# Kernel tuning notes

Measured on AMD Instinct MI355X. Metric: run time of the kernel, lower is better.

Reference implementation:

```python
import jax, jax.numpy as jnp
import numpy as np

NUM_HEADS = 8
MASK_RATE = 0.5


def setup_inputs() -> dict:
    key = jax.random.key(0)
    ks = jax.random.split(key, 6)
    B, N, C = 8, 1024, 256
    TABLE = 10
    att_embedding = jax.random.normal(ks[0], (B, N, C), dtype=jnp.float32)
    relation_position = jax.random.randint(ks[1], (B, N, N), 0, TABLE, dtype=jnp.int32)
    rel_len = jax.random.randint(ks[2], (B,), 0, 20, dtype=jnp.int32)
    W_qkv = jax.random.normal(ks[3], (C, 3 * C), dtype=jnp.float32) * (1.0 / np.sqrt(C))
    W_proj = jax.random.normal(ks[4], (C, C), dtype=jnp.float32) * (1.0 / np.sqrt(C))
    b_proj = jnp.zeros((C,), dtype=jnp.float32)
    bias_table = jax.random.normal(ks[5], (TABLE, NUM_HEADS), dtype=jnp.float32) * 0.02
    return {
        "att_embedding": att_embedding,
        "relation_position": relation_position,
        "rel_len": rel_len,
        "W_qkv": W_qkv,
        "W_proj": W_proj,
        "b_proj": b_proj,
        "bias_table": bias_table,
    }


def reference(att_embedding, relation_position, rel_len, W_qkv, W_proj, b_proj, bias_table):
    B, N, C = att_embedding.shape
    H = NUM_HEADS
    hd = C // H
    scale = hd ** -0.5

    # QKV projection (no bias): [B,N,3C] -> q,k,v each [B,H,N,hd]
    qkv = (att_embedding @ W_qkv).reshape(B, N, 3, H, hd)
    qkv = jnp.transpose(qkv, (2, 0, 3, 1, 4))
    q, k, v = qkv[0], qkv[1], qkv[2]

    # Attention scores [B,H,N,N]
    attn = jnp.einsum("bhnd,bhmd->bhnm", q, k) * scale

    # Relative position bias: gather [B,N,N,H] -> [B,H,N,N]
    pos_bias = jnp.transpose(bias_table[relation_position], (0, 3, 1, 2))

    # Mask bias: table row t gets -100 iff t > mask_len (mask_len+1 .. TABLE-1);
    # identical across heads -> compute as [B,1,N,N] instead of materializing [B,H,N,N].
    mask_len = (rel_len.astype(jnp.float32) * MASK_RATE).astype(jnp.int32)
    mask_bias = jnp.where(relation_position > mask_len[:, None, None], -100.0, 0.0)[:, None]

    attn = jax.nn.softmax(attn + pos_bias + mask_bias, axis=-1)

    # Weighted values -> [B,N,C] -> output projection
    x = jnp.einsum("bhnm,bhmd->bnhd", attn, v).reshape(B, N, C)
    x = x @ W_proj + b_proj
    return x
```

## Files before the change

### kernel.cpp

```cpp
#include <hip/hip_runtime.h>
#include <hip/hip_bf16.h>

typedef __bf16 bf16;
typedef __bf16 bf16x2 __attribute__((ext_vector_type(2)));
typedef __bf16 bf16x8 __attribute__((ext_vector_type(8)));
typedef float f32x4 __attribute__((ext_vector_type(4)));
typedef int i32x4 __attribute__((ext_vector_type(4)));

#define B_ 8
#define N_ 1024
#define C_ 256
#define H_ 8
#define C3_ 768
#define SCALE 0.17677669529663689f
#define FMAX 16.0f


__global__ __launch_bounds__(256) void prep(
    const float* __restrict__ Wqkv, const float* __restrict__ Wproj,
    bf16* __restrict__ Wq_tiled, bf16* __restrict__ Wp_tiled)
{
  int bb = blockIdx.x;
  int o = bb * 256 + threadIdx.x;
  if (bb < 768) {
    int kk = o & 31;
    int idx = o >> 5;
    int nr = idx & 63;
    int qq = idx >> 6;
    int nt = qq % 12, kt = qq / 12;
    int n = nt * 64 + nr, k = kt * 32 + kk;
    Wq_tiled[o] = (bf16)Wqkv[k * C3_ + n];
  } else {
    int p = o - 768 * 256;
    int kk = p & 31;
    int n = (p >> 5) & 255;
    int kt = p >> 13;
    int k = kt * 32 + kk;
    Wp_tiled[p] = (bf16)Wproj[k * C_ + n];
  }
}

__global__ __launch_bounds__(256) void gemm_qkv(
    const float* __restrict__ A, const bf16* __restrict__ Wq_tiled,
    bf16* __restrict__ q, bf16* __restrict__ kT, bf16* __restrict__ vT)
{
  __shared__ bf16 As[128][40];
  __shared__ bf16 Bts[128][40];
  __shared__ bf16 Vls[64][136];

  int tid = threadIdx.x;
  int wave = tid >> 6, lane = tid & 63, quad = lane >> 4, l16 = lane & 15;
  int m0 = blockIdx.x * 128, n0 = blockIdx.y * 128;
  int msub = (wave & 1) * 64, nsub = (wave >> 1) * 64;

  f32x4 acc[4][4] = {};

  int arow = tid >> 1, akc = (tid & 1) * 16;
  const float* aptr = A + (long)(m0 + arow) * C_ + akc;
  int bn = tid >> 1, bkc = (tid & 1) * 16;
  const bf16* bptr = Wq_tiled +
      ((long)(blockIdx.y * 2 + (bn >> 6)) * 2048 + (bn & 63) * 32 + bkc);

  float4 a0 = *reinterpret_cast<const float4*>(aptr);
  float4 a1 = *reinterpret_cast<const float4*>(aptr + 4);
  float4 a2 = *reinterpret_cast<const float4*>(aptr + 8);
  float4 a3 = *reinterpret_cast<const float4*>(aptr + 12);
  i32x4 bv0 = *reinterpret_cast<const i32x4*>(bptr);
  i32x4 bv1 = *reinterpret_cast<const i32x4*>(bptr + 8);

  for (int kt = 0; kt < 8; ++kt) {
    __syncthreads();
    {
      bf16 at[16] = {(bf16)a0.x, (bf16)a0.y, (bf16)a0.z, (bf16)a0.w,
                     (bf16)a1.x, (bf16)a1.y, (bf16)a1.z, (bf16)a1.w,
                     (bf16)a2.x, (bf16)a2.y, (bf16)a2.z, (bf16)a2.w,
                     (bf16)a3.x, (bf16)a3.y, (bf16)a3.z, (bf16)a3.w};
      *reinterpret_cast<bf16x8*>(&As[arow][akc]) = *reinterpret_cast<bf16x8*>(at);
      *reinterpret_cast<bf16x8*>(&As[arow][akc + 8]) = *reinterpret_cast<bf16x8*>(at + 8);
      *reinterpret_cast<i32x4*>(&Bts[bn][bkc]) = bv0;
      *reinterpret_cast<i32x4*>(&Bts[bn][bkc + 8]) = bv1;
    }
    __syncthreads();

    if (kt < 7) {
      int kn = (kt + 1) * 32;
      a0 = *reinterpret_cast<const float4*>(aptr + kn);
      a1 = *reinterpret_cast<const float4*>(aptr + kn + 4);
      a2 = *reinterpret_cast<const float4*>(aptr + kn + 8);
      a3 = *reinterpret_cast<const float4*>(aptr + kn + 12);
      bv0 = *reinterpret_cast<const i32x4*>(bptr + (long)(kt + 1) * 24576);
      bv1 = *reinterpret_cast<const i32x4*>(bptr + (long)(kt + 1) * 24576 + 8);
    }

    bf16x8 af[4], bfr[4];
#pragma unroll
    for (int mi = 0; mi < 4; ++mi)
      af[mi] = *reinterpret_cast<const bf16x8*>(&As[msub + mi * 16 + l16][quad * 8]);
#pragma unroll
    for (int ni = 0; ni < 4; ++ni)
      bfr[ni] = *reinterpret_cast<const bf16x8*>(&Bts[nsub + ni * 16 + l16][quad * 8]);
#pragma unroll
    for (int mi = 0; mi < 4; ++mi)
#pragma unroll
      for (int ni = 0; ni < 4; ++ni)
        acc[mi][ni] = __builtin_amdgcn_mfma_f32_16x16x32_bf16(af[mi], bfr[ni], acc[mi][ni], 0, 0, 0);
  }

  if (n0 < 256) {
#pragma unroll
    for (int mi = 0; mi < 4; ++mi)
#pragma unroll
      for (int ni = 0; ni < 4; ++ni)
#pragma unroll
        for (int r = 0; r < 4; ++r) {
          int row = m0 + msub + mi * 16 + quad * 4 + r;
          int col = n0 + nsub + ni * 16 + l16;
          q[(long)row * 256 + col] = (bf16)(acc[mi][ni][r] * SCALE);
        }
  } else if (n0 < 512) {
#pragma unroll
    for (int mi = 0; mi < 4; ++mi)
#pragma unroll
      for (int ni = 0; ni < 4; ++ni)
#pragma unroll
        for (int r = 0; r < 4; ++r) {
          int row = m0 + msub + mi * 16 + quad * 4 + r;
          int c = n0 + nsub + ni * 16 + l16 - 256;
          int b = row >> 10, n = row & 1023;
          int h = c >> 5, d = c & 31;
          kT[(((long)(b * H_ + h)) * N_ + n) * 32 + d] = (bf16)acc[mi][ni][r];
        }
  } else {
    int b = m0 >> 10;
#pragma unroll
    for (int ch = 0; ch < 2; ++ch) {
      __syncthreads();
      if ((nsub >> 6) == ch) {
#pragma unroll
        for (int mi = 0; mi < 4; ++mi)
#pragma unroll
          for (int ni = 0; ni < 4; ++ni)
#pragma unroll
            for (int r = 0; r < 4; ++r) {
              int cc = ni * 16 + l16;
              int nn = msub + mi * 16 + quad * 4 + r;
              int np = (nn & 96) | (2 * (nn & 15)) | ((nn >> 4) & 1);
              Vls[cc][np] = (bf16)acc[mi][ni][r];
            }
      }
      __syncthreads();
      int cc = tid >> 2, nseg = (tid & 3) * 32;
      long base = ((long)(b * C_ + (n0 - 512) + ch * 64 + cc)) * N_ + (m0 & 1023) + nseg;
#pragma unroll
      for (int j = 0; j < 4; ++j)
        *reinterpret_cast<i32x4*>(vT + base + j * 8) =
            *reinterpret_cast<const i32x4*>(&Vls[cc][nseg + j * 8]);
    }
  }
}

__global__ __launch_bounds__(512) void flash_attn(
    const bf16* __restrict__ q, const bf16* __restrict__ kT,
    const bf16* __restrict__ vT, const int* __restrict__ rel,
    const int* __restrict__ rel_len, const float* __restrict__ btab,
    const bf16* __restrict__ Wp_tiled, const float* __restrict__ bias,
    float* __restrict__ out)
{
  __shared__ bf16 Vs[256][40];
  __shared__ unsigned RelsP[4][33];
  __shared__ bf16 Pls[H_][16 * 40];
  __shared__ float btl[H_][16];
  __shared__ bf16 attL[16][264];

  int tid = threadIdx.x;
  int h = tid >> 6, lane = tid & 63, quad = lane >> 4, l16 = lane & 15;
  int b = blockIdx.y, i0 = blockIdx.x * 16;
  long bN = (long)b * N_;

  int mask_len = (int)((float)rel_len[b] * 0.5f);
  if (tid < 80) {
    int t = tid >> 3, hh = tid & 7;
    btl[hh][t] = btab[t * H_ + hh] + (t > mask_len ? -100.f : 0.f) - FMAX;
  }

  bf16x8 qf = *reinterpret_cast<const bf16x8*>(
      q + (bN + i0 + l16) * 256 + h * 32 + quad * 8);

  const bf16* kbase = kT + ((long)(b * H_ + h)) * N_ * 32 + quad * 8;
  int vrow = tid >> 1, voff = (tid & 1) * 16;
  const bf16* vgp = vT + ((long)b * C_ + vrow) * N_ + voff;
  int rg = (tid >> 5) & 3, rcol = tid & 31;
  const int* rgp = rel + (bN + i0 + rg * 4) * N_ + rcol;

  bf16x8 kf0 = *reinterpret_cast<const bf16x8*>(kbase + (long)l16 * 32);
  bf16x8 kf1 = *reinterpret_cast<const bf16x8*>(kbase + (long)(16 + l16) * 32);
  bf16x8 vr0 = *reinterpret_cast<const bf16x8*>(vgp);
  bf16x8 vr1 = *reinterpret_cast<const bf16x8*>(vgp + 8);
  int rr0 = 0, rr1 = 0, rr2 = 0, rr3 = 0;
  if (tid < 128) {
    rr0 = rgp[0]; rr1 = rgp[N_]; rr2 = rgp[2 * N_]; rr3 = rgp[3 * N_];
  }

  f32x4 oacc[2] = {};
  float l_part[4] = {0.f, 0.f, 0.f, 0.f};

  for (int j0 = 0; j0 < N_; j0 += 32) {
    __syncthreads();
    *reinterpret_cast<bf16x8*>(&Vs[vrow][voff]) = vr0;
    *reinterpret_cast<bf16x8*>(&Vs[vrow][voff + 8]) = vr1;
    if (tid < 128)
      RelsP[rg][rcol] = (unsigned)rr0 | ((unsigned)rr1 << 8) |
                        ((unsigned)rr2 << 16) | ((unsigned)rr3 << 24);
    __syncthreads();

    int jn = j0 + 32; jn = (jn < N_) ? jn : 0;
    bf16x8 kn0 = *reinterpret_cast<const bf16x8*>(kbase + (long)(jn + l16) * 32);
    bf16x8 kn1 = *reinterpret_cast<const bf16x8*>(kbase + (long)(jn + 16 + l16) * 32);
    vr0 = *reinterpret_cast<const bf16x8*>(vgp + jn);
    vr1 = *reinterpret_cast<const bf16x8*>(vgp + jn + 8);
    if (tid < 128) {
      rr0 = rgp[jn]; rr1 = rgp[N_ + jn];
      rr2 = rgp[2 * N_ + jn]; rr3 = rgp[3 * N_ + jn];
    }

    f32x4 z = {};
    f32x4 s0 = __builtin_amdgcn_mfma_f32_16x16x32_bf16(qf, kf0, z, 0, 0, 0);
    f32x4 s1 = __builtin_amdgcn_mfma_f32_16x16x32_bf16(qf, kf1, z, 0, 0, 0);
    kf0 = kn0; kf1 = kn1;

    unsigned w0 = RelsP[quad][l16];
    unsigned w1 = RelsP[quad][16 + l16];
#pragma unroll
    for (int r = 0; r < 4; ++r) {
      int il = quad * 4 + r;
      int rv0 = (w0 >> (8 * r)) & 255;
      int rv1 = (w1 >> (8 * r)) & 255;
      float p0 = __expf(s0[r] + btl[h][rv0]);
      float p1 = __expf(s1[r] + btl[h][rv1]);
      l_part[r] += p0 + p1;
      bf16x2 pp = {(bf16)p0, (bf16)p1};
      *reinterpret_cast<bf16x2*>(&Pls[h][il * 40 + l16 * 2]) = pp;
    }
    asm volatile("s_waitcnt lgkmcnt(0)" ::: "memory");
    bf16x8 pf = *reinterpret_cast<const bf16x8*>(&Pls[h][l16 * 40 + quad * 8]);
    bf16x8 vf0 = *reinterpret_cast<const bf16x8*>(&Vs[h * 32 + l16][quad * 8]);
    bf16x8 vf1 = *reinterpret_cast<const bf16x8*>(&Vs[h * 32 + 16 + l16][quad * 8]);
    oacc[0] = __builtin_amdgcn_mfma_f32_16x16x32_bf16(pf, vf0, oacc[0], 0, 0, 0);
    oacc[1] = __builtin_amdgcn_mfma_f32_16x16x32_bf16(pf, vf1, oacc[1], 0, 0, 0);
  }

#pragma unroll
  for (int r = 0; r < 4; ++r) {
    float l = l_part[r];
#pragma unroll
    for (int m = 1; m < 16; m <<= 1) l += __shfl_xor(l, m);
    float inv = 1.f / l;
    attL[quad * 4 + r][h * 32 + l16] = (bf16)(oacc[0][r] * inv);
    attL[quad * 4 + r][h * 32 + 16 + l16] = (bf16)(oacc[1][r] * inv);
  }
  __syncthreads();

  f32x4 pacc[2] = {};
  const bf16* wp = Wp_tiled + ((h * 32 + l16) * 32 + quad * 8);
#pragma unroll
  for (int kt = 0; kt < 8; ++kt) {
    bf16x8 afr = *reinterpret_cast<const bf16x8*>(&attL[l16][kt * 32 + quad * 8]);
    bf16x8 b0 = *reinterpret_cast<const bf16x8*>(wp + kt * 8192);
    bf16x8 b1 = *reinterpret_cast<const bf16x8*>(wp + kt * 8192 + 512);
    pacc[0] = __builtin_amdgcn_mfma_f32_16x16x32_bf16(afr, b0, pacc[0], 0, 0, 0);
    pacc[1] = __builtin_amdgcn_mfma_f32_16x16x32_bf16(afr, b1, pacc[1], 0, 0, 0);
  }
  float bi0 = bias[h * 32 + l16];
  float bi1 = bias[h * 32 + 16 + l16];
#pragma unroll
  for (int r = 0; r < 4; ++r) {
    long rowoff = (bN + i0 + quad * 4 + r) * C_ + h * 32;
    out[rowoff + l16] = pacc[0][r] + bi0;
    out[rowoff + 16 + l16] = pacc[1][r] + bi1;
  }
}

extern "C" void kernel_launch(void* const* d_in, const int* in_sizes, int n_in,
                              void* d_out, int out_size, void* d_ws, size_t ws_size,
                              hipStream_t stream) {
  const float* X     = (const float*)d_in[0];
  const int*   rel   = (const int*)d_in[1];
  const int*   rlen  = (const int*)d_in[2];
  const float* Wqkv  = (const float*)d_in[3];
  const float* Wproj = (const float*)d_in[4];
  const float* bproj = (const float*)d_in[5];
  const float* btab  = (const float*)d_in[6];
  float* out = (float*)d_out;

  char* ws = (char*)d_ws;
  bf16* Wq_tiled = (bf16*)ws;
  bf16* Wp_tiled = (bf16*)(ws + 393216);
  bf16* q  = (bf16*)(ws + 524288);
  bf16* kT = (bf16*)(ws + 524288 + 4194304);
  bf16* vT = (bf16*)(ws + 524288 + 2 * 4194304);

  prep<<<dim3(1024), 256, 0, stream>>>(Wqkv, Wproj, Wq_tiled, Wp_tiled);
  gemm_qkv<<<dim3(8192 / 128, C3_ / 128), 256, 0, stream>>>(X, Wq_tiled, q, kT, vT);
  flash_attn<<<dim3(N_ / 16, B_), 512, 0, stream>>>(
      q, kT, vT, rel, rlen, btab, Wp_tiled, bproj, out);
}
```

Before: 140.1 us.

## Halve QKV GEMM N-tile, fold log2e into scale, replicate bias LUT, coalesce prep

After: 151.0 us. 1.08x slower.

```diff
diff --git a/kernel.cpp b/kernel.cpp
--- a/kernel.cpp
+++ b/kernel.cpp
@@ -12,7 +12,7 @@
 #define C_ 256
 #define H_ 8
 #define C3_ 768
-#define SCALE 0.17677669529663689f
+#define QS 0.25500398f
 #define FMAX 16.0f
 
 
@@ -20,23 +20,17 @@
     const float* __restrict__ Wqkv, const float* __restrict__ Wproj,
     bf16* __restrict__ Wq_tiled, bf16* __restrict__ Wp_tiled)
 {
-  int bb = blockIdx.x;
-  int o = bb * 256 + threadIdx.x;
-  if (bb < 768) {
-    int kk = o & 31;
-    int idx = o >> 5;
-    int nr = idx & 63;
-    int qq = idx >> 6;
-    int nt = qq % 12, kt = qq / 12;
-    int n = nt * 64 + nr, k = kt * 32 + kk;
-    Wq_tiled[o] = (bf16)Wqkv[k * C3_ + n];
+  int o = blockIdx.x * 256 + threadIdx.x;
+  if (blockIdx.x < 768) {
+    int k = o / C3_, n = o % C3_;
+    float v = Wqkv[o];
+    int kt = k >> 5, kk = k & 31, nt = n >> 6, nr = n & 63;
+    Wq_tiled[kt * 24576 + nt * 2048 + nr * 32 + kk] = (bf16)v;
   } else {
     int p = o - 768 * 256;
-    int kk = p & 31;
-    int n = (p >> 5) & 255;
-    int kt = p >> 13;
-    int k = kt * 32 + kk;
-    Wp_tiled[p] = (bf16)Wproj[k * C_ + n];
+    int k = p >> 8, n = p & 255;
+    float v = Wproj[p];
+    Wp_tiled[(k >> 5) * 8192 + n * 32 + (k & 31)] = (bf16)v;
   }
 }
 
@@ -45,28 +39,26 @@
     bf16* __restrict__ q, bf16* __restrict__ kT, bf16* __restrict__ vT)
 {
   __shared__ bf16 As[128][40];
-  __shared__ bf16 Bts[128][40];
+  __shared__ bf16 Bts[64][40];
   __shared__ bf16 Vls[64][136];
 
   int tid = threadIdx.x;
   int wave = tid >> 6, lane = tid & 63, quad = lane >> 4, l16 = lane & 15;
-  int m0 = blockIdx.x * 128, n0 = blockIdx.y * 128;
-  int msub = (wave & 1) * 64, nsub = (wave >> 1) * 64;
-
-  f32x4 acc[4][4] = {};
+  int m0 = blockIdx.x * 128, by = blockIdx.y;
+  int msub = (wave & 1) * 64, nsub = (wave >> 1) * 32;
+
+  f32x4 acc[4][2] = {};
 
   int arow = tid >> 1, akc = (tid & 1) * 16;
   const float* aptr = A + (long)(m0 + arow) * C_ + akc;
-  int bn = tid >> 1, bkc = (tid & 1) * 16;
-  const bf16* bptr = Wq_tiled +
-      ((long)(blockIdx.y * 2 + (bn >> 6)) * 2048 + (bn & 63) * 32 + bkc);
+  int bn = tid >> 2, bkc = (tid & 3) * 8;
+  const bf16* bptr = Wq_tiled + ((long)by * 2048 + bn * 32 + bkc);
 
   float4 a0 = *reinterpret_cast<const float4*>(aptr);
   float4 a1 = *reinterpret_cast<const float4*>(aptr + 4);
   float4 a2 = *reinterpret_cast<const float4*>(aptr + 8);
   float4 a3 = *reinterpret_cast<const float4*>(aptr + 12);
-  i32x4 bv0 = *reinterpret_cast<const i32x4*>(bptr);
-  i32x4 bv1 = *reinterpret_cast<const i32x4*>(bptr + 8);
+  i32x4 bv = *reinterpret_cast<const i32x4*>(bptr);
 
   for (int kt = 0; kt < 8; ++kt) {
     __syncthreads();
@@ -77,8 +69,7 @@
                      (bf16)a3.x, (bf16)a3.y, (bf16)a3.z, (bf16)a3.w};
       *reinterpret_cast<bf16x8*>(&As[arow][akc]) = *reinterpret_cast<bf16x8*>(at);
       *reinterpret_cast<bf16x8*>(&As[arow][akc + 8]) = *reinterpret_cast<bf16x8*>(at + 8);
-      *reinterpret_cast<i32x4*>(&Bts[bn][bkc]) = bv0;
-      *reinterpret_cast<i32x4*>(&Bts[bn][bkc + 8]) = bv1;
+      *reinterpret_cast<i32x4*>(&Bts[bn][bkc]) = bv;
     }
     __syncthreads();
 
@@ -88,74 +79,68 @@
       a1 = *reinterpret_cast<const float4*>(aptr + kn + 4);
       a2 = *reinterpret_cast<const float4*>(aptr + kn + 8);
       a3 = *reinterpret_cast<const float4*>(aptr + kn + 12);
-      bv0 = *reinterpret_cast<const i32x4*>(bptr + (long)(kt + 1) * 24576);
-      bv1 = *reinterpret_cast<const i32x4*>(bptr + (long)(kt + 1) * 24576 + 8);
-    }
-
-    bf16x8 af[4], bfr[4];
+      bv = *reinterpret_cast<const i32x4*>(bptr + (long)(kt + 1) * 24576);
+    }
+
+    bf16x8 af[4], bfr[2];
 #pragma unroll
     for (int mi = 0; mi < 4; ++mi)
       af[mi] = *reinterpret_cast<const bf16x8*>(&As[msub + mi * 16 + l16][quad * 8]);
 #pragma unroll
-    for (int ni = 0; ni < 4; ++ni)
+    for (int ni = 0; ni < 2; ++ni)
       bfr[ni] = *reinterpret_cast<const bf16x8*>(&Bts[nsub + ni * 16 + l16][quad * 8]);
 #pragma unroll
     for (int mi = 0; mi < 4; ++mi)
 #pragma unroll
-      for (int ni = 0; ni < 4; ++ni)
+      for (int ni = 0; ni < 2; ++ni)
         acc[mi][ni] = __builtin_amdgcn_mfma_f32_16x16x32_bf16(af[mi], bfr[ni], acc[mi][ni], 0, 0, 0);
   }
 
-  if (n0 < 256) {
-#pragma unroll
-    for (int mi = 0; mi < 4; ++mi)
-#pragma unroll
-      for (int ni = 0; ni < 4; ++ni)
+  if (by < 4) {
+#pragma unroll
+    for (int mi = 0; mi < 4; ++mi)
+#pragma unroll
+      for (int ni = 0; ni < 2; ++ni)
 #pragma unroll
         for (int r = 0; r < 4; ++r) {
           int row = m0 + msub + mi * 16 + quad * 4 + r;
-          int col = n0 + nsub + ni * 16 + l16;
-          q[(long)row * 256 + col] = (bf16)(acc[mi][ni][r] * SCALE);
+          int col = by * 64 + nsub + ni * 16 + l16;
+          q[(long)row * 256 + col] = (bf16)(acc[mi][ni][r] * QS);
         }
-  } else if (n0 < 512) {
-#pragma unroll
-    for (int mi = 0; mi < 4; ++mi)
-#pragma unroll
-      for (int ni = 0; ni < 4; ++ni)
+  } else if (by < 8) {
+#pragma unroll
+    for (int mi = 0; mi < 4; ++mi)
+#pragma unroll
+      for (int ni = 0; ni < 2; ++ni)
 #pragma unroll
         for (int r = 0; r < 4; ++r) {
           int row = m0 + msub + mi * 16 + quad * 4 + r;
-          int c = n0 + nsub + ni * 16 + l16 - 256;
+          int c = (by - 4) * 64 + nsub + ni * 16 + l16;
           int b = row >> 10, n = row & 1023;
           int h = c >> 5, d = c & 31;
           kT[(((long)(b * H_ + h)) * N_ + n) * 32 + d] = (bf16)acc[mi][ni][r];
         }
   } else {
     int b = m0 >> 10;
-#pragma unroll
-    for (int ch = 0; ch < 2; ++ch) {
-      __syncthreads();
-      if ((nsub >> 6) == ch) {
-#pragma unroll
-        for (int mi = 0; mi < 4; ++mi)
-#pragma unroll
-          for (int ni = 0; ni < 4; ++ni)
-#pragma unroll
-            for (int r = 0; r < 4; ++r) {
-              int cc = ni * 16 + l16;
-              int nn = msub + mi * 16 + quad * 4 + r;
-              int np = (nn & 96) | (2 * (nn & 15)) | ((nn >> 4) & 1);
-              Vls[cc][np] = (bf16)acc[mi][ni][r];
-            }
-      }
-      __syncthreads();
-      int cc = tid >> 2, nseg = (tid & 3) * 32;
-      long base = ((long)(b * C_ + (n0 - 512) + ch * 64 + cc)) * N_ + (m0 & 1023) + nseg;
-#pragma unroll
-      for (int j = 0; j < 4; ++j)
-        *reinterpret_cast<i32x4*>(vT + base + j * 8) =
-            *reinterpret_cast<const i32x4*>(&Vls[cc][nseg + j * 8]);
-    }
+    __syncthreads();
+#pragma unroll
+    for (int mi = 0; mi < 4; ++mi)
+#pragma unroll
+      for (int ni = 0; ni < 2; ++ni)
+#pragma unroll
+        for (int r = 0; r < 4; ++r) {
+          int cc = nsub + ni * 16 + l16;
+          int nn = msub + mi * 16 + quad * 4 + r;
+          int np = (nn & 96) | (2 * (nn & 15)) | ((nn >> 4) & 1);
+          Vls[cc][np] = (bf16)acc[mi][ni][r];
+        }
+    __syncthreads();
+    int cc = tid >> 2, nseg = (tid & 3) * 32;
+    long base = ((long)(b * C_ + (by - 8) * 64 + cc)) * N_ + (m0 & 1023) + nseg;
+#pragma unroll
+    for (int j = 0; j < 4; ++j)
+      *reinterpret_cast<i32x4*>(vT + base + j * 8) =
+          *reinterpret_cast<const i32x4*>(&Vls[cc][nseg + j * 8]);
   }
 }
 
@@ -169,7 +154,7 @@
   __shared__ bf16 Vs[256][40];
   __shared__ unsigned RelsP[4][33];
   __shared__ bf16 Pls[H_][16 * 40];
-  __shared__ float btl[H_][16];
+  __shared__ float btlq[4][H_][17];
   __shared__ bf16 attL[16][264];
 
   int tid = threadIdx.x;
@@ -178,9 +163,10 @@
   long bN = (long)b * N_;
 
   int mask_len = (int)((float)rel_len[b] * 0.5f);
-  if (tid < 80) {
-    int t = tid >> 3, hh = tid & 7;
-    btl[hh][t] = btab[t * H_ + hh] + (t > mask_len ? -100.f : 0.f) - FMAX;
+  if (tid < 320) {
+    int cp = tid / 80, rem = tid % 80, t = rem >> 3, hh = rem & 7;
+    btlq[cp][hh][t] =
+        (btab[t * H_ + hh] + (t > mask_len ? -100.f : 0.f) - FMAX) * 1.44269504f;
   }
 
   bf16x8 qf = *reinterpret_cast<const bf16x8*>(
@@ -235,8 +221,8 @@
       int il = quad * 4 + r;
       int rv0 = (w0 >> (8 * r)) & 255;
       int rv1 = (w1 >> (8 * r)) & 255;
-      float p0 = __expf(s0[r] + btl[h][rv0]);
-      float p1 = __expf(s1[r] + btl[h][rv1]);
+      float p0 = exp2f(s0[r] + btlq[quad][h][rv0]);
+      float p1 = exp2f(s1[r] + btlq[quad][h][rv1]);
       l_part[r] += p0 + p1;
       bf16x2 pp = {(bf16)p0, (bf16)p1};
       *reinterpret_cast<bf16x2*>(&Pls[h][il * 40 + l16 * 2]) = pp;
@@ -300,7 +286,7 @@
   bf16* vT = (bf16*)(ws + 524288 + 2 * 4194304);
 
   prep<<<dim3(1024), 256, 0, stream>>>(Wqkv, Wproj, Wq_tiled, Wp_tiled);
-  gemm_qkv<<<dim3(8192 / 128, C3_ / 128), 256, 0, stream>>>(X, Wq_tiled, q, kT, vT);
+  gemm_qkv<<<dim3(64, 12), 256, 0, stream>>>(X, Wq_tiled, q, kT, vT);
   flash_attn<<<dim3(N_ / 16, B_), 512, 0, stream>>>(
       q, kT, vT, rel, rlen, btab, Wp_tiled, bproj, out);
 }
```
